# Optimization experiments

Measured on AMD Instinct MI355X. Metric: run time of the kernel, lower is better.

The kernel has to match this reference:

```python
import jax, jax.numpy as jnp
import numpy as np

N_NODES = 50000
N_EDGES = 1600000
D_FEAT = 512
FILTERS = 256
NUM_CLASSES = 16


def setup_inputs() -> dict:
    key = jax.random.key(0)
    k = jax.random.split(key, 6)
    x = jax.random.normal(k[0], (N_NODES, D_FEAT), dtype=jnp.float32)
    W1 = jax.random.normal(k[1], (D_FEAT, FILTERS), dtype=jnp.float32) * (1.0 / np.sqrt(D_FEAT))
    W2 = jax.random.normal(k[2], (FILTERS, NUM_CLASSES), dtype=jnp.float32) * (1.0 / np.sqrt(FILTERS))
    edge_weight = jax.random.uniform(k[3], (N_EDGES,), dtype=jnp.float32)
    edge_src = jax.random.randint(k[4], (N_EDGES,), 0, N_NODES, dtype=jnp.int32)
    edge_dst = jax.random.randint(k[5], (N_EDGES,), 0, N_NODES, dtype=jnp.int32)
    return {"x": x, "W1": W1, "W2": W2, "edge_weight": edge_weight,
            "edge_src": edge_src, "edge_dst": edge_dst}


def _propagate(h, edge_src, edge_dst, edge_weight):
    # sparse A @ h: out[dst] += w * h[src]
    msgs = edge_weight[:, None] * h[edge_src]          # [E, F]
    return jax.ops.segment_sum(msgs, edge_dst, num_segments=N_NODES)


def reference(x, W1, W2, edge_weight, edge_src, edge_dst):
    # Dropout layers are identity at inference (training=False).
    # Layer 1: relu(A @ (X @ W1))
    h = jax.nn.relu(_propagate(x @ W1, edge_src, edge_dst, edge_weight))
    # Layer 2: softmax(A @ (H @ W2))
    logits = _propagate(h @ W2, edge_src, edge_dst, edge_weight)
    return jax.nn.softmax(logits, axis=-1)
```

## Files before the change

### kernel.cpp

```cpp
#include <hip/hip_runtime.h>

#define N_NODES 50000
#define N_EDGES 1600000
#define D_FEAT 512
#define FILTERS 256
#define NUM_CLASSES 16
#define NXCD 8

typedef __bf16 bf16x8 __attribute__((ext_vector_type(8)));
typedef float f32x4 __attribute__((ext_vector_type(4)));
typedef _Float16 half4 __attribute__((ext_vector_type(4)));
typedef _Float16 f16x8 __attribute__((ext_vector_type(8)));

#define GLOAD_LDS16(g, l)                                                  \
  __builtin_amdgcn_global_load_lds(                                        \
      (const __attribute__((address_space(1))) unsigned int*)(g),          \
      (__attribute__((address_space(3))) unsigned int*)(l), 16, 0, 0)

__global__ __launch_bounds__(256) void hist8_kernel(
    const int* __restrict__ edst, int* __restrict__ deg8,
    const float* __restrict__ W1, __bf16* __restrict__ Wth,
    __bf16* __restrict__ Wtl) {
  const int e = blockIdx.x * 256 + threadIdx.x;
  if (e < D_FEAT * FILTERS) {
    const float v = W1[e];
    const int k = e >> 8;
    const int n = e & 255;
    const __bf16 h = (__bf16)v;
    Wth[n * D_FEAT + k] = h;
    Wtl[n * D_FEAT + k] = (__bf16)(v - (float)h);
  }
  if (e >= N_EDGES) return;
  const int x = (e >> 8) & (NXCD - 1);
  atomicAdd(&deg8[x * N_NODES + edst[e]], 1);
}

#define SCAN_NB 196
__global__ __launch_bounds__(256) void scan_blocks_kernel(
    const int* __restrict__ deg8, int* __restrict__ row_ptr,
    int* __restrict__ bsum) {
  __shared__ int s[256];
  const int i = blockIdx.x * 256 + threadIdx.x;
  int v = 0;
  if (i < N_NODES) {
#pragma unroll
    for (int x = 0; x < NXCD; ++x) v += deg8[x * N_NODES + i];
  }
  s[threadIdx.x] = v;
  __syncthreads();
  for (int off = 1; off < 256; off <<= 1) {
    const int t = (threadIdx.x >= off) ? s[threadIdx.x - off] : 0;
    __syncthreads();
    s[threadIdx.x] += t;
    __syncthreads();
  }
  if (i < N_NODES) row_ptr[i] = s[threadIdx.x] - v;
  if (threadIdx.x == 255) bsum[blockIdx.x] = s[255];
}

__global__ __launch_bounds__(256) void scan_add_cursor8_kernel(
    int* __restrict__ row_ptr, const int* __restrict__ bsum,
    const int* __restrict__ deg8, int* __restrict__ cursor8) {
  __shared__ int wsum[4];
  const int lane = threadIdx.x & 63;
  const int wave = threadIdx.x >> 6;
  int v = (threadIdx.x < blockIdx.x) ? bsum[threadIdx.x] : 0;
#pragma unroll
  for (int off = 32; off >= 1; off >>= 1) v += __shfl_xor(v, off, 64);
  if (lane == 0) wsum[wave] = v;
  __syncthreads();
  const int boff = wsum[0] + wsum[1] + wsum[2] + wsum[3];

  const int i = blockIdx.x * 256 + threadIdx.x;
  if (i < N_NODES) {
    int run = row_ptr[i] + boff;
    row_ptr[i] = run;
#pragma unroll
    for (int x = 0; x < NXCD; ++x) {
      cursor8[x * N_NODES + i] = run;
      run += deg8[x * N_NODES + i];
    }
  }
  if (i == 0) row_ptr[N_NODES] = N_EDGES;
}

#define G1_BX 391
#define G1_BLOCKS (G1_BX * 2)
__global__ __launch_bounds__(256) void gemm1_fill_kernel(
    const float* __restrict__ A, const __bf16* __restrict__ Bh,
    const __bf16* __restrict__ Bl, _Float16* __restrict__ C,
    const int* __restrict__ esrc, const int* __restrict__ edst,
    const float* __restrict__ ew, int* __restrict__ cursor8,
    uint2* __restrict__ meta8) {
  __shared__ __bf16 sAh[128 * 32];
  __shared__ __bf16 sAl[128 * 32];
  __shared__ __bf16 sBh[128 * 32];
  __shared__ __bf16 sBl[128 * 32];

  if (blockIdx.x >= G1_BLOCKS) {
    const int e = (blockIdx.x - G1_BLOCKS) * 256 + threadIdx.x;
    if (e < N_EDGES) {
      const int x = (e >> 8) & (NXCD - 1);
      const int d = edst[e];
      const int pos = atomicAdd(&cursor8[x * N_NODES + d], 1);
      meta8[pos] = make_uint2((unsigned)esrc[e] | ((unsigned)(d & 15) << 16),
                              __float_as_uint(ew[e]));
    }
    return;
  }

  const int K = D_FEAT;
  const int tid = threadIdx.x;
  const int wave = tid >> 6;
  const int lane = tid & 63;
  const int wm = (wave >> 1) * 64;
  const int wn = (wave & 1) * 64;
  const int m0 = (blockIdx.x % G1_BX) * 128;
  const int n0 = (blockIdx.x / G1_BX) * 128;

  const int arow = tid >> 1;
  const int aks = (tid & 1) * 16;
  int am = m0 + arow;
  if (am >= N_NODES) am = N_NODES - 1;
  const float* aptr = A + (size_t)am * K + aks;

  const int lr = lane >> 2;
  const int lc = (lane & 3) * 8;
  const int fm = lane & 15;
  const int fq = lane >> 4;

  f32x4 acc[4][4] = {};

  for (int k0 = 0; k0 < K; k0 += 32) {
    const float4* ap = (const float4*)(aptr + k0);
    const float4 a0 = ap[0], a1 = ap[1], a2 = ap[2], a3 = ap[3];

    __syncthreads();

#pragma unroll
    for (int i = 0; i < 2; ++i) {
      const int row = wave * 32 + i * 16;
      GLOAD_LDS16(Bh + (size_t)(n0 + row + lr) * K + k0 + lc, sBh + row * 32);
      GLOAD_LDS16(Bl + (size_t)(n0 + row + lr) * K + k0 + lc, sBl + row * 32);
    }

    float va[16] = {a0.x, a0.y, a0.z, a0.w, a1.x, a1.y, a1.z, a1.w,
                    a2.x, a2.y, a2.z, a2.w, a3.x, a3.y, a3.z, a3.w};
    __bf16 hh[16], ll[16];
#pragma unroll
    for (int i = 0; i < 16; ++i) {
      const __bf16 h = (__bf16)va[i];
      hh[i] = h;
      ll[i] = (__bf16)(va[i] - (float)h);
    }
    *(bf16x8*)(sAh + arow * 32 + aks) = *(bf16x8*)&hh[0];
    *(bf16x8*)(sAh + arow * 32 + aks + 8) = *(bf16x8*)&hh[8];
    *(bf16x8*)(sAl + arow * 32 + aks) = *(bf16x8*)&ll[0];
    *(bf16x8*)(sAl + arow * 32 + aks + 8) = *(bf16x8*)&ll[8];

    __syncthreads();

    bf16x8 fah[4], fal[4], fbh[4], fbl[4];
#pragma unroll
    for (int t = 0; t < 4; ++t) {
      const int moff = (wm + t * 16 + fm) * 32 + fq * 8;
      fah[t] = *(const bf16x8*)(sAh + moff);
      fal[t] = *(const bf16x8*)(sAl + moff);
      const int noff = (wn + t * 16 + fm) * 32 + fq * 8;
      fbh[t] = *(const bf16x8*)(sBh + noff);
      fbl[t] = *(const bf16x8*)(sBl + noff);
    }
#pragma unroll
    for (int i = 0; i < 4; ++i)
#pragma unroll
      for (int j = 0; j < 4; ++j)
        acc[i][j] = __builtin_amdgcn_mfma_f32_16x16x32_bf16(fah[i], fbh[j],
                                                            acc[i][j], 0, 0, 0);
#pragma unroll
    for (int i = 0; i < 4; ++i)
#pragma unroll
      for (int j = 0; j < 4; ++j)
        acc[i][j] = __builtin_amdgcn_mfma_f32_16x16x32_bf16(fah[i], fbl[j],
                                                            acc[i][j], 0, 0, 0);
#pragma unroll
    for (int i = 0; i < 4; ++i)
#pragma unroll
      for (int j = 0; j < 4; ++j)
        acc[i][j] = __builtin_amdgcn_mfma_f32_16x16x32_bf16(fal[i], fbh[j],
                                                            acc[i][j], 0, 0, 0);
  }

#pragma unroll
  for (int ti = 0; ti < 4; ++ti) {
#pragma unroll
    for (int r = 0; r < 4; ++r) {
      const int m = m0 + wm + ti * 16 + fq * 4 + r;
      if (m < N_NODES) {
#pragma unroll
        for (int tj = 0; tj < 4; ++tj) {
          const int n = n0 + wn + tj * 16 + fm;
          C[(size_t)m * FILTERS + n] = (_Float16)acc[ti][tj][r];
        }
      }
    }
  }
}

__global__ __launch_bounds__(256) void gather1_gemm2_kernel(
    const _Float16* __restrict__ xw1, const int* __restrict__ row_ptr,
    const uint2* __restrict__ meta8, const float* __restrict__ W2,
    _Float16* __restrict__ h2) {
  __shared__ float red[4][16][17];
  const int wave = threadIdx.x >> 6;
  const int lane = threadIdx.x & 63;
  const int node = blockIdx.x * 4 + wave;
  const int beg = row_ptr[node];
  const int end = row_ptr[node + 1];

  float acc[4] = {};
  const half4* __restrict__ xw1v = (const half4*)xw1;

  for (int c0 = beg; c0 < end; c0 += 64) {
    const int cnt = min(64, end - c0);
    const uint2 mv = meta8[c0 + ((lane < cnt) ? lane : 0)];

    for (int j = 0; j < cnt; j += 8) {
      int srcs[8];
      float ws[8];
#pragma unroll
      for (int u = 0; u < 8; ++u) {
        const int live = (j + u < cnt);
        const int l = live ? (j + u) : 0;
        srcs[u] = __builtin_amdgcn_readlane((int)mv.x, l) & 0xFFFF;
        const int wb = __builtin_amdgcn_readlane((int)mv.y, l);
        ws[u] = live ? __int_as_float(wb) : 0.f;
      }
      half4 v[8];
#pragma unroll
      for (int u = 0; u < 8; ++u)
        v[u] = xw1v[(unsigned)srcs[u] * 64u + (unsigned)lane];
#pragma unroll
      for (int u = 0; u < 8; ++u)
#pragma unroll
        for (int i = 0; i < 4; ++i)
          acc[i] = fmaf(ws[u], (float)v[u][i], acc[i]);
    }
  }

  float r[4];
#pragma unroll
  for (int i = 0; i < 4; ++i) r[i] = fmaxf(acc[i], 0.f);

  float p[16] = {};
#pragma unroll
  for (int j = 0; j < 4; ++j) {
    const float4* wr = (const float4*)(W2 + (size_t)(lane * 4 + j) * NUM_CLASSES);
#pragma unroll
    for (int c4 = 0; c4 < 4; ++c4) {
      const float4 wv = wr[c4];
      p[c4 * 4 + 0] = fmaf(r[j], wv.x, p[c4 * 4 + 0]);
      p[c4 * 4 + 1] = fmaf(r[j], wv.y, p[c4 * 4 + 1]);
      p[c4 * 4 + 2] = fmaf(r[j], wv.z, p[c4 * 4 + 2]);
      p[c4 * 4 + 3] = fmaf(r[j], wv.w, p[c4 * 4 + 3]);
    }
  }

#pragma unroll
  for (int off = 32; off >= 16; off >>= 1)
#pragma unroll
    for (int i = 0; i < 16; ++i) p[i] += __shfl_xor(p[i], off, 64);

  if (lane < 16) {
#pragma unroll
    for (int i = 0; i < 16; ++i) red[wave][lane][i] = p[i];
  }
  if (lane < 16) {
    float sum = 0.f;
#pragma unroll
    for (int i = 0; i < 16; ++i) sum += red[wave][i][lane];
    h2[(size_t)node * NUM_CLASSES + lane] = (_Float16)sum;
  }
}

__global__ __launch_bounds__(256) void gather2_mfma_kernel(
    const _Float16* __restrict__ h2, const int* __restrict__ row_ptr,
    const uint2* __restrict__ meta8, float* __restrict__ out) {
  __shared__ _Float16 lds[4][16][72];
  const int wave = threadIdx.x >> 6;
  const int lane = threadIdx.x & 63;
  const int tile = blockIdx.x * 4 + wave;
  if (tile >= N_NODES / 16) return;
  const int t0 = tile * 16;
  const int beg = row_ptr[t0];
  const int end = row_ptr[t0 + 16];

  const int cls = lane & 15;
  const int kq = lane >> 4;
  const int erow = lane >> 1;
  const int part = lane & 1;

  f32x4 acc = {0.f, 0.f, 0.f, 0.f};
  _Float16* myl = &lds[wave][0][0];

  if (beg < end) {
    const int last = end - 1;
    int e = beg + lane;
    uint2 m = meta8[(e <= last) ? e : last];
    float wv = (e <= last) ? __uint_as_float(m.y) : 0.f;

    for (int c0 = beg; c0 < end; c0 += 64) {
      uint2 mn = m;
      float wn = 0.f;
      const int c1 = c0 + 64;
      if (c1 < end) {
        const int en = c1 + lane;
        mn = meta8[(en <= last) ? en : last];
        wn = (en <= last) ? __uint_as_float(mn.y) : 0.f;
      }

      const int se0 = __shfl((int)m.x, erow, 64) & 0xFFFF;
      const int se1 = __shfl((int)m.x, 32 + erow, 64) & 0xFFFF;
      const f16x8 r0 =
          *(const f16x8*)(h2 + (size_t)se0 * NUM_CLASSES + part * 8);
      const f16x8 r1 =
          *(const f16x8*)(h2 + (size_t)se1 * NUM_CLASSES + part * 8);

      f16x8 a0, a1;
#pragma unroll
      for (int j = 0; j < 8; ++j) {
        const int ei = kq * 8 + j;
        const int p0 = __shfl((int)m.x, ei, 64);
        const float w0 = __shfl(wv, ei, 64);
        a0[j] = (((p0 >> 16) & 15) == cls) ? (_Float16)w0 : (_Float16)0.f;
        const int p1 = __shfl((int)m.x, 32 + ei, 64);
        const float w1 = __shfl(wv, 32 + ei, 64);
        a1[j] = (((p1 >> 16) & 15) == cls) ? (_Float16)w1 : (_Float16)0.f;
      }

#pragma unroll
      for (int j = 0; j < 8; ++j) myl[(part * 8 + j) * 72 + erow] = r0[j];
#pragma unroll
      for (int j = 0; j < 8; ++j) myl[(part * 8 + j) * 72 + 32 + erow] = r1[j];

      const f16x8 b0 = *(const f16x8*)(myl + cls * 72 + kq * 8);
      const f16x8 b1 = *(const f16x8*)(myl + cls * 72 + 32 + kq * 8);

      acc = __builtin_amdgcn_mfma_f32_16x16x32_f16(a0, b0, acc, 0, 0, 0);
      acc = __builtin_amdgcn_mfma_f32_16x16x32_f16(a1, b1, acc, 0, 0, 0);

      m = mn;
      wv = wn;
    }
  }

#pragma unroll
  for (int r = 0; r < 4; ++r) {
    const float a = acc[r];
    float mx = a;
#pragma unroll
    for (int off = 8; off >= 1; off >>= 1)
      mx = fmaxf(mx, __shfl_xor(mx, off, 16));
    const float ex = __expf(a - mx);
    float sm = ex;
#pragma unroll
    for (int off = 8; off >= 1; off >>= 1) sm += __shfl_xor(sm, off, 16);
    out[(size_t)(t0 + kq * 4 + r) * NUM_CLASSES + cls] = ex / sm;
  }
}

extern "C" void kernel_launch(void* const* d_in, const int* in_sizes, int n_in,
                              void* d_out, int out_size, void* d_ws,
                              size_t ws_size, hipStream_t stream) {
  const float* x = (const float*)d_in[0];
  const float* W1 = (const float*)d_in[1];
  const float* W2 = (const float*)d_in[2];
  const float* ew = (const float*)d_in[3];
  const int* esrc = (const int*)d_in[4];
  const int* edst = (const int*)d_in[5];
  float* out = (float*)d_out;

  _Float16* xw1 = (_Float16*)d_ws;
  _Float16* h2 = xw1 + (size_t)N_NODES * FILTERS;
  int* row_ptr = (int*)(h2 + (size_t)N_NODES * NUM_CLASSES);
  int* deg8 = row_ptr + (N_NODES + 1);
  int* cursor8 = deg8 + NXCD * N_NODES;
  uint2* meta8 = (uint2*)(((uintptr_t)(cursor8 + NXCD * N_NODES) + 15) &
                          ~(uintptr_t)15);
  __bf16* w1th = (__bf16*)(meta8 + N_EDGES);
  __bf16* w1tl = w1th + D_FEAT * FILTERS;
  int* bsum = (int*)(w1tl + D_FEAT * FILTERS);

  hipMemsetAsync(deg8, 0, NXCD * N_NODES * sizeof(int), stream);
  hist8_kernel<<<(N_EDGES + 255) / 256, 256, 0, stream>>>(edst, deg8, W1,
                                                          w1th, w1tl);
  scan_blocks_kernel<<<SCAN_NB, 256, 0, stream>>>(deg8, row_ptr, bsum);
  scan_add_cursor8_kernel<<<SCAN_NB, 256, 0, stream>>>(row_ptr, bsum, deg8,
                                                       cursor8);

  gemm1_fill_kernel<<<G1_BLOCKS + (N_EDGES + 255) / 256, 256, 0, stream>>>(
      x, w1th, w1tl, xw1, esrc, edst, ew, cursor8, meta8);

  gather1_gemm2_kernel<<<N_NODES / 4, 256, 0, stream>>>(xw1, row_ptr, meta8,
                                                        W2, h2);

  gather2_mfma_kernel<<<(N_NODES / 16 + 3) / 4, 256, 0, stream>>>(h2, row_ptr,
                                                                  meta8, out);
}
```

Before: 489.7 us.

## Use 64x256 GEMM tiles and fuse scan kernels with cooperative grid sync

The GEMM1 tiling changes from 128x128 blocks, where each block covered half of N, to 64-row blocks that cover all 256 output columns. This means each x row is read and split into bf16 hi/lo once instead of twice, cutting global reads of the fp32 input. Separately, the two scan kernels merge into one cooperative kernel that uses grid.sync, removing a launch and the row_ptr round trip. The risk is that the larger B tile in LDS lowers occupancy, and that the cooperative launch adds its own overhead.

```diff
diff --git a/kernel.cpp b/kernel.cpp
--- a/kernel.cpp
+++ b/kernel.cpp
@@ -1,4 +1,5 @@
 #include <hip/hip_runtime.h>
+#include <hip/hip_cooperative_groups.h>
 
 #define N_NODES 50000
 #define N_EDGES 1600000
@@ -36,11 +37,14 @@
 }
 
 #define SCAN_NB 196
-__global__ __launch_bounds__(256) void scan_blocks_kernel(
+__global__ __launch_bounds__(256) void scan_coop_kernel(
     const int* __restrict__ deg8, int* __restrict__ row_ptr,
-    int* __restrict__ bsum) {
+    int* __restrict__ bsum, int* __restrict__ cursor8) {
+  cooperative_groups::grid_group grid = cooperative_groups::this_grid();
   __shared__ int s[256];
+  __shared__ int wsum[4];
   const int i = blockIdx.x * 256 + threadIdx.x;
+
   int v = 0;
   if (i < N_NODES) {
 #pragma unroll
@@ -54,26 +58,21 @@
     s[threadIdx.x] += t;
     __syncthreads();
   }
-  if (i < N_NODES) row_ptr[i] = s[threadIdx.x] - v;
+  const int excl = s[threadIdx.x] - v;
   if (threadIdx.x == 255) bsum[blockIdx.x] = s[255];
-}
-
-__global__ __launch_bounds__(256) void scan_add_cursor8_kernel(
-    int* __restrict__ row_ptr, const int* __restrict__ bsum,
-    const int* __restrict__ deg8, int* __restrict__ cursor8) {
-  __shared__ int wsum[4];
+  grid.sync();
+
   const int lane = threadIdx.x & 63;
   const int wave = threadIdx.x >> 6;
-  int v = (threadIdx.x < blockIdx.x) ? bsum[threadIdx.x] : 0;
-#pragma unroll
-  for (int off = 32; off >= 1; off >>= 1) v += __shfl_xor(v, off, 64);
-  if (lane == 0) wsum[wave] = v;
+  int bv = (threadIdx.x < blockIdx.x) ? bsum[threadIdx.x] : 0;
+#pragma unroll
+  for (int off = 32; off >= 1; off >>= 1) bv += __shfl_xor(bv, off, 64);
+  if (lane == 0) wsum[wave] = bv;
   __syncthreads();
   const int boff = wsum[0] + wsum[1] + wsum[2] + wsum[3];
 
-  const int i = blockIdx.x * 256 + threadIdx.x;
   if (i < N_NODES) {
-    int run = row_ptr[i] + boff;
+    int run = excl + boff;
     row_ptr[i] = run;
 #pragma unroll
     for (int x = 0; x < NXCD; ++x) {
@@ -84,18 +83,17 @@
   if (i == 0) row_ptr[N_NODES] = N_EDGES;
 }
 
-#define G1_BX 391
-#define G1_BLOCKS (G1_BX * 2)
+#define G1_BLOCKS 782
 __global__ __launch_bounds__(256) void gemm1_fill_kernel(
     const float* __restrict__ A, const __bf16* __restrict__ Bh,
     const __bf16* __restrict__ Bl, _Float16* __restrict__ C,
     const int* __restrict__ esrc, const int* __restrict__ edst,
     const float* __restrict__ ew, int* __restrict__ cursor8,
     uint2* __restrict__ meta8) {
-  __shared__ __bf16 sAh[128 * 32];
-  __shared__ __bf16 sAl[128 * 32];
-  __shared__ __bf16 sBh[128 * 32];
-  __shared__ __bf16 sBl[128 * 32];
+  __shared__ __bf16 sAh[64 * 32];
+  __shared__ __bf16 sAl[64 * 32];
+  __shared__ __bf16 sBh[256 * 32];
+  __shared__ __bf16 sBl[256 * 32];
 
   if (blockIdx.x >= G1_BLOCKS) {
     const int e = (blockIdx.x - G1_BLOCKS) * 256 + threadIdx.x;
@@ -113,13 +111,11 @@
   const int tid = threadIdx.x;
   const int wave = tid >> 6;
   const int lane = tid & 63;
-  const int wm = (wave >> 1) * 64;
-  const int wn = (wave & 1) * 64;
-  const int m0 = (blockIdx.x % G1_BX) * 128;
-  const int n0 = (blockIdx.x / G1_BX) * 128;
-
-  const int arow = tid >> 1;
-  const int aks = (tid & 1) * 16;
+  const int wn = wave * 64;
+  const int m0 = blockIdx.x * 64;
+
+  const int arow = tid >> 2;
+  const int aks = (tid & 3) * 8;
   int am = m0 + arow;
   if (am >= N_NODES) am = N_NODES - 1;
   const float* aptr = A + (size_t)am * K + aks;
@@ -133,37 +129,34 @@
 
   for (int k0 = 0; k0 < K; k0 += 32) {
     const float4* ap = (const float4*)(aptr + k0);
-    const float4 a0 = ap[0], a1 = ap[1], a2 = ap[2], a3 = ap[3];
+    const float4 a0 = ap[0], a1 = ap[1];
 
     __syncthreads();
 
 #pragma unroll
-    for (int i = 0; i < 2; ++i) {
-      const int row = wave * 32 + i * 16;
-      GLOAD_LDS16(Bh + (size_t)(n0 + row + lr) * K + k0 + lc, sBh + row * 32);
-      GLOAD_LDS16(Bl + (size_t)(n0 + row + lr) * K + k0 + lc, sBl + row * 32);
-    }
-
-    float va[16] = {a0.x, a0.y, a0.z, a0.w, a1.x, a1.y, a1.z, a1.w,
-                    a2.x, a2.y, a2.z, a2.w, a3.x, a3.y, a3.z, a3.w};
-    __bf16 hh[16], ll[16];
-#pragma unroll
-    for (int i = 0; i < 16; ++i) {
+    for (int i = 0; i < 4; ++i) {
+      const int row = wn + i * 16;
+      GLOAD_LDS16(Bh + (size_t)(row + lr) * K + k0 + lc, sBh + row * 32);
+      GLOAD_LDS16(Bl + (size_t)(row + lr) * K + k0 + lc, sBl + row * 32);
+    }
+
+    float va[8] = {a0.x, a0.y, a0.z, a0.w, a1.x, a1.y, a1.z, a1.w};
+    __bf16 hh[8], ll[8];
+#pragma unroll
+    for (int i = 0; i < 8; ++i) {
       const __bf16 h = (__bf16)va[i];
       hh[i] = h;
       ll[i] = (__bf16)(va[i] - (float)h);
     }
     *(bf16x8*)(sAh + arow * 32 + aks) = *(bf16x8*)&hh[0];
-    *(bf16x8*)(sAh + arow * 32 + aks + 8) = *(bf16x8*)&hh[8];
     *(bf16x8*)(sAl + arow * 32 + aks) = *(bf16x8*)&ll[0];
-    *(bf16x8*)(sAl + arow * 32 + aks + 8) = *(bf16x8*)&ll[8];
 
     __syncthreads();
 
     bf16x8 fah[4], fal[4], fbh[4], fbl[4];
 #pragma unroll
     for (int t = 0; t < 4; ++t) {
-      const int moff = (wm + t * 16 + fm) * 32 + fq * 8;
+      const int moff = (t * 16 + fm) * 32 + fq * 8;
       fah[t] = *(const bf16x8*)(sAh + moff);
       fal[t] = *(const bf16x8*)(sAl + moff);
       const int noff = (wn + t * 16 + fm) * 32 + fq * 8;
@@ -194,11 +187,11 @@
   for (int ti = 0; ti < 4; ++ti) {
 #pragma unroll
     for (int r = 0; r < 4; ++r) {
-      const int m = m0 + wm + ti * 16 + fq * 4 + r;
+      const int m = m0 + ti * 16 + fq * 4 + r;
       if (m < N_NODES) {
 #pragma unroll
         for (int tj = 0; tj < 4; ++tj) {
-          const int n = n0 + wn + tj * 16 + fm;
+          const int n = wn + tj * 16 + fm;
           C[(size_t)m * FILTERS + n] = (_Float16)acc[ti][tj][r];
         }
       }
@@ -393,9 +386,11 @@
   hipMemsetAsync(deg8, 0, NXCD * N_NODES * sizeof(int), stream);
   hist8_kernel<<<(N_EDGES + 255) / 256, 256, 0, stream>>>(edst, deg8, W1,
                                                           w1th, w1tl);
-  scan_blocks_kernel<<<SCAN_NB, 256, 0, stream>>>(deg8, row_ptr, bsum);
-  scan_add_cursor8_kernel<<<SCAN_NB, 256, 0, stream>>>(row_ptr, bsum, deg8,
-                                                       cursor8);
+
+  void* sargs[] = {(void*)&deg8, (void*)&row_ptr, (void*)&bsum,
+                   (void*)&cursor8};
+  hipLaunchCooperativeKernel((const void*)scan_coop_kernel, dim3(SCAN_NB),
+                             dim3(256), sargs, 0, stream);
 
   gemm1_fill_kernel<<<G1_BLOCKS + (N_EDGES + 255) / 256, 256, 0, stream>>>(
       x, w1th, w1tl, xw1, esrc, edst, ew, cursor8, meta8);
```

After: 540.2 us. +10.3%, slower.
